# Performance work log

Hardware: AMD Instinct MI355X
Metric: run time of the kernel (lower is better)

Reference implementation:

```python
import jax, jax.numpy as jnp
import numpy as np

L = 6          # n_layers
D = 128        # patch_dim
COND = 128     # cond_dim
HID = 256      # hidden (fixed default in AffineCoupling)
DIN = D // 2 + COND  # 192, input dim of coupling net


def setup_inputs() -> dict:
    key = jax.random.key(0)
    ks = jax.random.split(key, 8)
    x = jax.random.normal(ks[0], (512, 128, D), dtype=jnp.float32)
    cond = jax.random.normal(ks[1], (512, COND), dtype=jnp.float32)
    # per-layer weights stacked over L; stored [in, out] (torch Linear transposed)
    W1 = jax.random.normal(ks[2], (L, DIN, HID), dtype=jnp.float32) * 0.05
    b1 = jnp.zeros((L, HID), dtype=jnp.float32)
    W2 = jax.random.normal(ks[3], (L, HID, HID), dtype=jnp.float32) * 0.05
    b2 = jnp.zeros((L, HID), dtype=jnp.float32)
    W3 = jax.random.normal(ks[4], (L, HID, D), dtype=jnp.float32) * 0.05
    b3 = jnp.zeros((L, D), dtype=jnp.float32)
    return {"x": x, "cond": cond, "W1": W1, "b1": b1, "W2": W2, "b2": b2, "W3": W3, "b3": b3}


def reference(x, cond, W1, b1, W2, b2, W3, b3):
    B, P, Dd = x.shape
    # cond is shared across patches: broadcast to [B, P, COND]
    condb = jnp.broadcast_to(cond[:, None, :], (B, P, cond.shape[-1]))
    z = x
    logdet = jnp.zeros((B,), dtype=x.dtype)
    for i in range(W1.shape[0]):
        x1, x2 = jnp.split(z, 2, axis=-1)                       # [B,P,D/2] each
        h = jnp.concatenate([x1, condb], axis=-1)               # [B,P,DIN]
        h = jax.nn.relu(jnp.einsum('bpi,ih->bph', h, W1[i]) + b1[i])
        h = jax.nn.relu(jnp.einsum('bph,hk->bpk', h, W2[i]) + b2[i])
        st = jnp.einsum('bpk,kd->bpd', h, W3[i]) + b3[i]        # [B,P,D]
        s, t = jnp.split(st, 2, axis=-1)
        s = jnp.tanh(s) * 0.5
        y2 = x2 * jnp.exp(s) + t
        z = jnp.concatenate([x1, y2], axis=-1)[..., ::-1]        # flip feature dim
        logdet = logdet + s.sum(axis=(1, 2))
    return z, logdet
```

## Files before the change

kernel.cpp:

```cpp
#include <hip/hip_runtime.h>
#include <stdint.h>

#define NLAYERS 6
#define DD      128
#define CONDD   128
#define HID     256
#define DIN     192
#define TM      64
#define NTHR    512

typedef __attribute__((ext_vector_type(4))) float f32x4;
typedef __attribute__((ext_vector_type(2))) float f32x2;
typedef __attribute__((ext_vector_type(8))) short short8;

#define G1_KS 2
#define G2_KS 8
#define G3_KS 8
#define G1_FR (G1_KS*16)
#define G2_FR (G2_KS*16)
#define G3_FR (G3_KS*8)
#define FR_L  (G1_FR+G2_FR+G3_FR)
#define EL_L  (FR_L*512)
#define G2_OFF (G1_FR*512)
#define G3_OFF ((G1_FR+G2_FR)*512)

__device__ __forceinline__ short f2bf(float f) {
  uint32_t u = __builtin_bit_cast(uint32_t, f);
  u += 0x7fffu + ((u >> 16) & 1u);
  return (short)(u >> 16);
}
__device__ __forceinline__ uint32_t pack2bf(float a, float b) {
  uint32_t ua = __builtin_bit_cast(uint32_t, a);
  ua += 0x7fffu + ((ua >> 16) & 1u);
  uint32_t ub = __builtin_bit_cast(uint32_t, b);
  ub += 0x7fffu + ((ub >> 16) & 1u);
  return (ua >> 16) | (ub & 0xffff0000u);
}
__device__ __forceinline__ int SW(int row) { return ((row & 7) << 4) ^ ((row & 8) << 2); }
__device__ __forceinline__ int kinv(int p) {
  return (p & ~63) | (p & 32) | ((p & 1) << 4) | ((p >> 1) & 15);
}

__global__ void prep_weights(const float* __restrict__ W1,
                             const float* __restrict__ W2,
                             const float* __restrict__ W3,
                             short* __restrict__ wp)
{
  int t = blockIdx.x * 256 + threadIdx.x;
  int lay  = t / (FR_L * 64);
  int rem  = t - lay * (FR_L * 64);
  int frag = rem >> 6;
  int lane = rem & 63;
  const float* src;
  int N, f2, dstbase, nfr, perm;
  if (frag < G1_FR) {
    f2 = frag;                  src = W1 + (size_t)lay * DIN * HID; N = HID; dstbase = 0;      nfr = 16; perm = 0;
  } else if (frag < G1_FR + G2_FR) {
    f2 = frag - G1_FR;          src = W2 + (size_t)lay * HID * HID; N = HID; dstbase = G2_OFF; nfr = 16; perm = 1;
  } else {
    f2 = frag - (G1_FR + G2_FR);src = W3 + (size_t)lay * HID * DD;  N = DD;  dstbase = G3_OFF; nfr = 8;  perm = 1;
  }
  int ks = f2 / nfr, nf = f2 - ks * nfr;
  int n  = nf * 16 + (lane & 15);
  int k0 = ks * 32 + (lane >> 4) * 8;
  short8 v;
#pragma unroll
  for (int j = 0; j < 8; ++j) {
    int k = perm ? kinv(k0 + j) : (k0 + j);
    v[j] = f2bf(src[(size_t)k * N + n]);
  }
  *(short8*)(wp + (size_t)lay * EL_L + dstbase + ((size_t)f2 * 64 + lane) * 8) = v;
}

__global__ void prep_c1(const float* __restrict__ cond, const float* __restrict__ W1,
                        const float* __restrict__ b1, float* __restrict__ c1)
{
  int lay = blockIdx.x >> 9;
  int b   = blockIdx.x & 511;
  int h   = threadIdx.x;
  const float* wb = W1 + (size_t)lay * DIN * HID + 64 * HID + h;
  const float* cb = cond + b * CONDD;
  float acc = b1[lay * HID + h];
#pragma unroll 4
  for (int c = 0; c < CONDD; ++c) acc = fmaf(cb[c], wb[(size_t)c * HID], acc);
  c1[((size_t)lay * 512 + b) * HID + h] = acc;
}

__global__ __launch_bounds__(NTHR, 4)
void flow_kernel(const float* __restrict__ x,
                 const float* __restrict__ c1g, const float* __restrict__ b2g,
                 const float* __restrict__ b3g, const short* __restrict__ wp,
                 float* __restrict__ outz, float* __restrict__ outld)
{
  __shared__ alignas(16) short bufA[TM * 64];
  __shared__ alignas(16) short bufB[TM * HID];
  __shared__ alignas(16) short bufC[TM * HID];
  __shared__ float red[8];

  const int tid  = threadIdx.x;
  const int wave = tid >> 6;
  const int lane = tid & 63;
  const int l15  = lane & 15;
  const int l4   = lane >> 4;
  const int mh   = wave >> 2;
  const int nq   = wave & 3;
  const int t0   = blockIdx.x * TM;
  const int batch = t0 >> 7;
  float* stf = (float*)bufB;

  float zlo[8], zhi[8];
  int d = lane;
  {
    const float* xb = x + (size_t)t0 * DD + wave * DD + lane;
#pragma unroll
    for (int j = 0; j < 8; ++j) {
      zlo[j] = xb[j * 8 * DD];
      zhi[j] = xb[j * 8 * DD + 64];
    }
#pragma unroll
    for (int j = 0; j < 8; ++j) {
      int m = wave + 8 * j;
      *(short*)((char*)bufA + (((m * 64 + d) * 2) ^ SW(m))) = f2bf(zlo[j]);
    }
  }
  float ldsum = 0.f;
  const f32x4 vzero = {0.f, 0.f, 0.f, 0.f};
  __syncthreads();

#pragma unroll 1
  for (int lay = 0; lay < NLAYERS; ++lay) {
    const short* wl = wp + (size_t)lay * EL_L;

    {
      f32x4 acc[2][4];
#pragma unroll
      for (int m2 = 0; m2 < 2; ++m2)
#pragma unroll
        for (int nf = 0; nf < 4; ++nf) acc[m2][nf] = vzero;
#pragma unroll
      for (int ks = 0; ks < G1_KS; ++ks) {
        short8 bb[4];
#pragma unroll
        for (int nf = 0; nf < 4; ++nf)
          bb[nf] = *(const short8*)(wl + (((ks * 16 + 4 * nq + nf) * 64 + lane) * 8));
#pragma unroll
        for (int m2 = 0; m2 < 2; ++m2) {
          int row = 32 * mh + 16 * m2 + l15;
          short8 a = *(const short8*)((const char*)bufA +
                       (((row * 64 + ks * 32 + l4 * 8) * 2) ^ SW(row)));
#pragma unroll
          for (int nf = 0; nf < 4; ++nf)
            acc[m2][nf] = __builtin_amdgcn_mfma_f32_16x16x32_bf16(a, bb[nf], acc[m2][nf], 0, 0, 0);
        }
      }
      const float* c1row = c1g + ((size_t)lay * 512 + batch) * HID;
#pragma unroll
      for (int h = 0; h < 2; ++h) {
        int c0 = 64 * nq + 32 * h + l15;
        float bias0 = c1row[c0], bias1 = c1row[c0 + 16];
#pragma unroll
        for (int m2 = 0; m2 < 2; ++m2)
#pragma unroll
          for (int r = 0; r < 4; ++r) {
            int row = 32 * mh + 16 * m2 + 4 * l4 + r;
            float v0 = fmaxf(acc[m2][2 * h][r] + bias0, 0.f);
            float v1 = fmaxf(acc[m2][2 * h + 1][r] + bias1, 0.f);
            *(uint32_t*)((char*)bufB +
              (((row * HID + 64 * nq + 32 * h + 2 * l15) * 2) ^ SW(row))) = pack2bf(v0, v1);
          }
      }
    }
    __syncthreads();

    {
      const short* wg = wl + G2_OFF;
      f32x4 acc[2][4];
#pragma unroll
      for (int m2 = 0; m2 < 2; ++m2)
#pragma unroll
        for (int nf = 0; nf < 4; ++nf) acc[m2][nf] = vzero;
#pragma unroll 2
      for (int ks = 0; ks < G2_KS; ++ks) {
        short8 bb[4];
#pragma unroll
        for (int nf = 0; nf < 4; ++nf)
          bb[nf] = *(const short8*)(wg + (((ks * 16 + 4 * nq + nf) * 64 + lane) * 8));
#pragma unroll
        for (int m2 = 0; m2 < 2; ++m2) {
          int row = 32 * mh + 16 * m2 + l15;
          short8 a = *(const short8*)((const char*)bufB +
                       (((row * HID + ks * 32 + l4 * 8) * 2) ^ SW(row)));
#pragma unroll
          for (int nf = 0; nf < 4; ++nf)
            acc[m2][nf] = __builtin_amdgcn_mfma_f32_16x16x32_bf16(a, bb[nf], acc[m2][nf], 0, 0, 0);
        }
      }
#pragma unroll
      for (int h = 0; h < 2; ++h) {
        int c0 = 64 * nq + 32 * h + l15;
        float bias0 = b2g[lay * HID + c0], bias1 = b2g[lay * HID + c0 + 16];
#pragma unroll
        for (int m2 = 0; m2 < 2; ++m2)
#pragma unroll
          for (int r = 0; r < 4; ++r) {
            int row = 32 * mh + 16 * m2 + 4 * l4 + r;
            float v0 = fmaxf(acc[m2][2 * h][r] + bias0, 0.f);
            float v1 = fmaxf(acc[m2][2 * h + 1][r] + bias1, 0.f);
            *(uint32_t*)((char*)bufC +
              (((row * HID + 64 * nq + 32 * h + 2 * l15) * 2) ^ SW(row))) = pack2bf(v0, v1);
          }
      }
    }
    __syncthreads();

    {
      f32x4 acc3[2][2];
#pragma unroll
      for (int m2 = 0; m2 < 2; ++m2) { acc3[m2][0] = vzero; acc3[m2][1] = vzero; }
#pragma unroll 2
      for (int ks = 0; ks < G3_KS; ++ks) {
        short8 bb[2];
#pragma unroll
        for (int nf = 0; nf < 2; ++nf)
          bb[nf] = *(const short8*)(wl + G3_OFF + (((ks * 8 + 2 * nq + nf) * 64 + lane) * 8));
#pragma unroll
        for (int m2 = 0; m2 < 2; ++m2) {
          int row = 32 * mh + 16 * m2 + l15;
          short8 a = *(const short8*)((const char*)bufC +
                       (((row * HID + ks * 32 + l4 * 8) * 2) ^ SW(row)));
          acc3[m2][0] = __builtin_amdgcn_mfma_f32_16x16x32_bf16(a, bb[0], acc3[m2][0], 0, 0, 0);
          acc3[m2][1] = __builtin_amdgcn_mfma_f32_16x16x32_bf16(a, bb[1], acc3[m2][1], 0, 0, 0);
        }
      }
      float bias0 = b3g[lay * DD + 32 * nq + l15];
      float bias1 = b3g[lay * DD + 32 * nq + 16 + l15];
#pragma unroll
      for (int m2 = 0; m2 < 2; ++m2)
#pragma unroll
        for (int r = 0; r < 4; ++r) {
          int row = 32 * mh + 16 * m2 + 4 * l4 + r;
          f32x2 val = {acc3[m2][0][r] + bias0, acc3[m2][1][r] + bias1};
          *(f32x2*)((char*)stf +
            (((row * DD + 32 * nq + 2 * l15) * 4) ^ (((row >> 2) & 1) << 6))) = val;
        }
    }
    __syncthreads();

    int ps = (d & 32) | ((d & 15) << 1) | ((d >> 4) & 1);
#pragma unroll
    for (int j = 0; j < 8; ++j) {
      int m = wave + 8 * j;
      int rsw = ((m >> 2) & 1) << 6;
      float sr = *(const float*)((const char*)stf + (((m * DD + ps) * 4) ^ rsw));
      float tt = *(const float*)((const char*)stf + (((m * DD + 64 + ps) * 4) ^ rsw));
      sr = fminf(fmaxf(sr, -8.f), 8.f);
      float e2 = __expf(2.f * sr);
      float s  = 0.5f * (e2 - 1.f) / (e2 + 1.f);
      ldsum += s;
      float y2 = fmaf(zhi[j], __expf(s), tt);
      zhi[j] = zlo[j];
      zlo[j] = y2;
    }
    d = 63 - d;
    if (lay < NLAYERS - 1) {
#pragma unroll
      for (int j = 0; j < 8; ++j) {
        int m = wave + 8 * j;
        *(short*)((char*)bufA + (((m * 64 + d) * 2) ^ SW(m))) = f2bf(zlo[j]);
      }
    }
    __syncthreads();
  }

  {
    float* ob = outz + (size_t)t0 * DD + wave * DD;
#pragma unroll
    for (int j = 0; j < 8; ++j) {
      ob[j * 8 * DD + d]      = zlo[j];
      ob[j * 8 * DD + 64 + d] = zhi[j];
    }
  }
#pragma unroll
  for (int off = 32; off > 0; off >>= 1) ldsum += __shfl_down(ldsum, off);
  if (lane == 0) red[wave] = ldsum;
  __syncthreads();
  if (tid == 0) {
    float s = 0.f;
#pragma unroll
    for (int w = 0; w < 8; ++w) s += red[w];
    atomicAdd(&outld[batch], s);
  }
}

extern "C" void kernel_launch(void* const* d_in, const int* in_sizes, int n_in,
                              void* d_out, int out_size, void* d_ws, size_t ws_size,
                              hipStream_t stream)
{
  (void)in_sizes; (void)n_in; (void)out_size; (void)ws_size;
  const float* x   = (const float*)d_in[0];
  const float* cnd = (const float*)d_in[1];
  const float* W1  = (const float*)d_in[2];
  const float* b1  = (const float*)d_in[3];
  const float* W2  = (const float*)d_in[4];
  const float* b2  = (const float*)d_in[5];
  const float* W3  = (const float*)d_in[6];
  const float* b3  = (const float*)d_in[7];
  float* outz  = (float*)d_out;
  float* outld = outz + (size_t)512 * 128 * 128;
  short* wp = (short*)d_ws;
  float* c1 = (float*)((char*)d_ws + (2u << 20));

  hipMemsetAsync(outld, 0, 512 * sizeof(float), stream);
  prep_weights<<<336, 256, 0, stream>>>(W1, W2, W3, wp);
  prep_c1<<<6 * 512, 256, 0, stream>>>(cnd, W1, b1, c1);
  flow_kernel<<<1024, NTHR, 0, stream>>>(x, c1, b2, b3, wp, outz, outld);
}
```

Before: 168.3 us.

## Apply coupling epilogue in MFMA registers with permuted W3 columns, drop LDS round-trip

```diff
diff --git a/kernel.cpp b/kernel.cpp
--- a/kernel.cpp
+++ b/kernel.cpp
@@ -10,7 +10,6 @@
 #define NTHR    512
 
 typedef __attribute__((ext_vector_type(4))) float f32x4;
-typedef __attribute__((ext_vector_type(2))) float f32x2;
 typedef __attribute__((ext_vector_type(8))) short short8;
 
 #define G1_KS 2
@@ -58,10 +57,18 @@
   } else if (frag < G1_FR + G2_FR) {
     f2 = frag - G1_FR;          src = W2 + (size_t)lay * HID * HID; N = HID; dstbase = G2_OFF; nfr = 16; perm = 1;
   } else {
-    f2 = frag - (G1_FR + G2_FR);src = W3 + (size_t)lay * HID * DD;  N = DD;  dstbase = G3_OFF; nfr = 8;  perm = 1;
+    f2 = frag - (G1_FR + G2_FR);src = W3 + (size_t)lay * HID * DD;  N = DD;  dstbase = G3_OFF; nfr = 8;  perm = 2;
   }
   int ks = f2 / nfr, nf = f2 - ks * nfr;
-  int n  = nf * 16 + (lane & 15);
+  int lv = lane & 15;
+  int n;
+  if (perm == 2) {
+    int g = nf >> 1, h = nf & 1;
+    int c = (lv < 8) ? 8 * g + lv : 48 - 8 * g + lv;
+    n = c + 64 * h;
+  } else {
+    n = nf * 16 + lv;
+  }
   int k0 = ks * 32 + (lane >> 4) * 8;
   short8 v;
 #pragma unroll
@@ -106,22 +113,27 @@
   const int nq   = wave & 3;
   const int t0   = blockIdx.x * TM;
   const int batch = t0 >> 7;
-  float* stf = (float*)bufB;
-
+
+  const int cT = (l15 < 8) ? 8 * nq + l15 : 48 - 8 * nq + l15;
   float zlo[8], zhi[8];
-  int d = lane;
   {
-    const float* xb = x + (size_t)t0 * DD + wave * DD + lane;
-#pragma unroll
-    for (int j = 0; j < 8; ++j) {
-      zlo[j] = xb[j * 8 * DD];
-      zhi[j] = xb[j * 8 * DD + 64];
-    }
-#pragma unroll
-    for (int j = 0; j < 8; ++j) {
-      int m = wave + 8 * j;
-      *(short*)((char*)bufA + (((m * 64 + d) * 2) ^ SW(m))) = f2bf(zlo[j]);
-    }
+    const float* xb = x + (size_t)t0 * DD;
+#pragma unroll
+    for (int m2 = 0; m2 < 2; ++m2)
+#pragma unroll
+      for (int r = 0; r < 4; ++r) {
+        int j = m2 * 4 + r;
+        int row = 32 * mh + 16 * m2 + 4 * l4 + r;
+        zlo[j] = xb[row * DD + cT];
+        zhi[j] = xb[row * DD + 64 + cT];
+      }
+#pragma unroll
+    for (int m2 = 0; m2 < 2; ++m2)
+#pragma unroll
+      for (int r = 0; r < 4; ++r) {
+        int row = 32 * mh + 16 * m2 + 4 * l4 + r;
+        *(short*)((char*)bufA + (((row * 64 + cT) * 2) ^ SW(row))) = f2bf(zlo[m2 * 4 + r]);
+      }
   }
   float ldsum = 0.f;
   const f32x4 vzero = {0.f, 0.f, 0.f, 0.f};
@@ -232,53 +244,49 @@
           acc3[m2][1] = __builtin_amdgcn_mfma_f32_16x16x32_bf16(a, bb[1], acc3[m2][1], 0, 0, 0);
         }
       }
-      float bias0 = b3g[lay * DD + 32 * nq + l15];
-      float bias1 = b3g[lay * DD + 32 * nq + 16 + l15];
+      float bias_s = b3g[lay * DD + cT];
+      float bias_t = b3g[lay * DD + 64 + cT];
 #pragma unroll
       for (int m2 = 0; m2 < 2; ++m2)
 #pragma unroll
         for (int r = 0; r < 4; ++r) {
-          int row = 32 * mh + 16 * m2 + 4 * l4 + r;
-          f32x2 val = {acc3[m2][0][r] + bias0, acc3[m2][1][r] + bias1};
-          *(f32x2*)((char*)stf +
-            (((row * DD + 32 * nq + 2 * l15) * 4) ^ (((row >> 2) & 1) << 6))) = val;
+          int j = m2 * 4 + r;
+          float sr = acc3[m2][0][r] + bias_s;
+          sr = fminf(fmaxf(sr, -8.f), 8.f);
+          float tt = acc3[m2][1][r] + bias_t;
+          float e2 = __expf(2.f * sr);
+          float s  = 0.5f * (e2 - 1.f) / (e2 + 1.f);
+          ldsum += s;
+          float y2 = fmaf(zhi[j], __expf(s), tt);
+          float py = __shfl_xor(y2, 15);
+          float pl = __shfl_xor(zlo[j], 15);
+          zlo[j] = py;
+          zhi[j] = pl;
         }
+      if (lay < NLAYERS - 1) {
+#pragma unroll
+        for (int m2 = 0; m2 < 2; ++m2)
+#pragma unroll
+          for (int r = 0; r < 4; ++r) {
+            int row = 32 * mh + 16 * m2 + 4 * l4 + r;
+            *(short*)((char*)bufA + (((row * 64 + cT) * 2) ^ SW(row))) = f2bf(zlo[m2 * 4 + r]);
+          }
+        __syncthreads();
+      }
     }
-    __syncthreads();
-
-    int ps = (d & 32) | ((d & 15) << 1) | ((d >> 4) & 1);
-#pragma unroll
-    for (int j = 0; j < 8; ++j) {
-      int m = wave + 8 * j;
-      int rsw = ((m >> 2) & 1) << 6;
-      float sr = *(const float*)((const char*)stf + (((m * DD + ps) * 4) ^ rsw));
-      float tt = *(const float*)((const char*)stf + (((m * DD + 64 + ps) * 4) ^ rsw));
-      sr = fminf(fmaxf(sr, -8.f), 8.f);
-      float e2 = __expf(2.f * sr);
-      float s  = 0.5f * (e2 - 1.f) / (e2 + 1.f);
-      ldsum += s;
-      float y2 = fmaf(zhi[j], __expf(s), tt);
-      zhi[j] = zlo[j];
-      zlo[j] = y2;
-    }
-    d = 63 - d;
-    if (lay < NLAYERS - 1) {
-#pragma unroll
-      for (int j = 0; j < 8; ++j) {
-        int m = wave + 8 * j;
-        *(short*)((char*)bufA + (((m * 64 + d) * 2) ^ SW(m))) = f2bf(zlo[j]);
-      }
-    }
-    __syncthreads();
   }
 
   {
-    float* ob = outz + (size_t)t0 * DD + wave * DD;
-#pragma unroll
-    for (int j = 0; j < 8; ++j) {
-      ob[j * 8 * DD + d]      = zlo[j];
-      ob[j * 8 * DD + 64 + d] = zhi[j];
-    }
+    float* ob = outz + (size_t)t0 * DD;
+#pragma unroll
+    for (int m2 = 0; m2 < 2; ++m2)
+#pragma unroll
+      for (int r = 0; r < 4; ++r) {
+        int j = m2 * 4 + r;
+        int row = 32 * mh + 16 * m2 + 4 * l4 + r;
+        ob[row * DD + cT]      = zlo[j];
+        ob[row * DD + 64 + cT] = zhi[j];
+      }
   }
 #pragma unroll
   for (int off = 32; off > 0; off >>= 1) ldsum += __shfl_down(ldsum, off);
```

Result: slower. 172.7 us (+2.6%).
